# Optimization experiments

Measured on AMD Instinct MI355X. Metric: run time of the kernel, lower is better.

Reference implementation:

```python
import jax, jax.numpy as jnp
import numpy as np

I, H, L, D, O = 256, 512, 2, 2, 8  # input, hidden, layers, directions, output


def _lstm_dir(x, h0, c0, w_ih, w_hh, b, reverse):
    """One LSTM direction. x: [S,B,in] -> hidden seq [S,B,H] (time-aligned)."""
    def step(carry, xt):
        h, c = carry
        gates = xt @ w_ih.T + h @ w_hh.T + b            # [B,4H], PyTorch gate order i,f,g,o
        i, f, g, o = jnp.split(gates, 4, axis=-1)
        c = jax.nn.sigmoid(f) * c + jax.nn.sigmoid(i) * jnp.tanh(g)
        h = jax.nn.sigmoid(o) * jnp.tanh(c)
        return (h, c), h
    _, ys = jax.lax.scan(step, (h0, c0), x, reverse=reverse)
    return ys


def setup_inputs() -> dict:
    key = jax.random.key(0)
    ks = jax.random.split(key, 32)
    s = 1.0 / np.sqrt(H)
    inp = {
        "input_seq": jax.random.normal(ks[0], (64, 512, I), jnp.float32),
        "h0": jax.random.normal(ks[1], (L * D, 64, H), jnp.float32),
        "c0": jax.random.normal(ks[2], (L * D, 64, H), jnp.float32),
    }
    k = 3
    for l in range(L):
        in_dim = I if l == 0 else H * D
        for d, tag in enumerate("fb"):
            inp[f"w_ih_{l}{tag}"] = jax.random.uniform(ks[k], (4 * H, in_dim), jnp.float32, -s, s); k += 1
            inp[f"w_hh_{l}{tag}"] = jax.random.uniform(ks[k], (4 * H, H), jnp.float32, -s, s); k += 1
            inp[f"b_{l}{tag}"] = jax.random.uniform(ks[k], (4 * H,), jnp.float32, -s, s); k += 1  # b_ih + b_hh combined
    inp["fc_w"] = jax.random.uniform(ks[k], (O, H * D), jnp.float32, -s, s); k += 1
    inp["fc_b"] = jax.random.uniform(ks[k], (O,), jnp.float32, -s, s)
    return inp


def reference(input_seq, h0, c0,
              w_ih_0f, w_hh_0f, b_0f, w_ih_0b, w_hh_0b, b_0b,
              w_ih_1f, w_hh_1f, b_1f, w_ih_1b, w_hh_1b, b_1b,
              fc_w, fc_b):
    x = jnp.transpose(input_seq, (1, 0, 2))  # [S,B,I] time-major
    params = [
        ((w_ih_0f, w_hh_0f, b_0f), (w_ih_0b, w_hh_0b, b_0b)),
        ((w_ih_1f, w_hh_1f, b_1f), (w_ih_1b, w_hh_1b, b_1b)),
    ]
    for l, (pf, pb) in enumerate(params):
        fwd = _lstm_dir(x, h0[2 * l], c0[2 * l], *pf, reverse=False)
        bwd = _lstm_dir(x, h0[2 * l + 1], c0[2 * l + 1], *pb, reverse=True)
        x = jnp.concatenate([fwd, bwd], axis=-1)  # [S,B,2H]
    last = x[-1]                                   # [B,2H] == output[:, -1, :]
    pred = last @ fc_w.T + fc_b                    # fc then slice last step (same math)
    return pred[None]                              # torch.stack([pred], dim=0) -> [1,B,O]
```

## Files before the change

kernel.cpp:

```cpp
#include <hip/hip_runtime.h>
#include <hip/hip_bf16.h>


typedef __attribute__((ext_vector_type(8))) __bf16 bf16x8;
typedef __attribute__((ext_vector_type(4))) float f32x4;

struct Params {
  const float *input_seq, *h0, *c0;
  const float *w_ih_0f, *w_hh_0f, *b_0f;
  const float *w_ih_0b, *w_hh_0b, *b_0b;
  const float *w_ih_1f, *w_hh_1f, *b_1f;
  const float *w_ih_1b, *w_hh_1b, *b_1b;
  const float *fc_w, *fc_b;
  float* out;
  unsigned* flags;
  unsigned* stepf;
  __bf16* xT;
  __bf16* Wp0f; __bf16* Wp0b;
  __bf16* Wp1f; __bf16* Wp1b;
  __bf16* y0;
  __bf16* y1f;
  __bf16* h1binit;
  __bf16* h1bout;
  float* bp;
};

__device__ __forceinline__ float sigm(float x) { return 1.f / (1.f + __expf(-x)); }
__device__ __forceinline__ float tanh_fast(float x) {
  return 1.f - 2.f / (1.f + __expf(2.f * x));
}
__device__ __forceinline__ void pin(bf16x8& v) { asm volatile("" : "+v"(v)); }

__device__ __forceinline__ void phase_barrier(unsigned* pf, int wg, int tid, unsigned phase) {
  __syncthreads();
  if (tid == 0) {
    __builtin_amdgcn_fence(__ATOMIC_RELEASE, "agent");
    __hip_atomic_store(pf + wg, phase, __ATOMIC_RELAXED, __HIP_MEMORY_SCOPE_AGENT);
  }
  bool ok;
  unsigned it = 0;
  do {
    unsigned v = __hip_atomic_load(pf + tid, __ATOMIC_RELAXED, __HIP_MEMORY_SCOPE_AGENT);
    ok = (v >= phase) || (++it > 200000u);
    if (!ok) __builtin_amdgcn_s_sleep(8);
  } while (!__syncthreads_and(ok));
  __builtin_amdgcn_fence(__ATOMIC_ACQUIRE, "agent");
}

__device__ __forceinline__ bool group_wait128(const unsigned* base, int lane,
                                              unsigned need, bool fast) {
  for (unsigned it = 0;; ++it) {
    unsigned v0 = __hip_atomic_load(base + (size_t)lane * 16, __ATOMIC_RELAXED,
                                    __HIP_MEMORY_SCOPE_AGENT);
    unsigned v1 = __hip_atomic_load(base + (size_t)(lane + 64) * 16, __ATOMIC_RELAXED,
                                    __HIP_MEMORY_SCOPE_AGENT);
    bool ok = (v0 >= need) && (v1 >= need);
    if (__ballot(ok) == ~0ull) break;
    if (it > 1000000u) return false;
    if (!fast) __builtin_amdgcn_s_sleep(1);
  }
  asm volatile("" ::: "memory");
  return true;
}

__device__ __forceinline__ void flag_store(unsigned* a, unsigned v, bool fast) {
  if (fast) __hip_atomic_store(a, v, __ATOMIC_RELAXED, __HIP_MEMORY_SCOPE_WORKGROUP);
  else      __hip_atomic_store(a, v, __ATOMIC_RELAXED, __HIP_MEMORY_SCOPE_AGENT);
}

__device__ __forceinline__ void pointwise_t2(f32x4 g4, float& c,
                                             __bf16* eptr, bool fast) {
  float cj = sigm(g4[1]) * c + sigm(g4[0]) * tanh_fast(g4[2]);
  c = cj;
  float h = sigm(g4[3]) * tanh_fast(cj);
  __bf16 hb = (__bf16)h;
  unsigned short hu; __builtin_memcpy(&hu, &hb, 2);
  if (fast)
    __hip_atomic_store((unsigned short*)eptr, hu,
                       __ATOMIC_RELAXED, __HIP_MEMORY_SCOPE_WORKGROUP);
  else
    __hip_atomic_store((unsigned short*)eptr, hu,
                       __ATOMIC_RELAXED, __HIP_MEMORY_SCOPE_AGENT);
}

__global__ __launch_bounds__(256, 1) void lstm_kernel(Params p) {
  const int tid  = threadIdx.x;
  const int wg   = blockIdx.x;
  const unsigned gtid = wg * 256 + tid;
  const int lane = tid & 63;
  const int wv   = tid >> 6;
  const int colq = lane & 15;
  const int quad = lane >> 4;

  __shared__ __bf16 wlds[32768];

  {
    unsigned xcd = __builtin_amdgcn_s_getreg(20 | (31 << 11));
    if (tid == 0) p.flags[512 + wg] = xcd;
  }
  {
    int row = gtid >> 1, half = gtid & 1;
    int t = row >> 6, b = row & 63;
    const float* src = p.input_seq + ((size_t)b * 512 + t) * 256 + half * 128;
    __bf16* dst = p.xT + (size_t)row * 256 + half * 128;
    for (int i = 0; i < 128; i += 8) {
      bf16x8 v;
      #pragma unroll
      for (int j = 0; j < 8; ++j) v[j] = (__bf16)src[i + j];
      *(bf16x8*)(dst + i) = v;
    }
  }
  for (unsigned task = gtid; task < 2u * 2048 * 6; task += 65536) {
    unsigned dir = task / (2048 * 6);
    unsigned rr = (task / 6) % 2048;
    unsigned ch = task % 6;
    unsigned R = (rr & 3) * 512 + (rr >> 2);
    const float* wih = dir ? p.w_ih_0b : p.w_ih_0f;
    const float* whh = dir ? p.w_hh_0b : p.w_hh_0f;
    __bf16* dst = (dir ? p.Wp0b : p.Wp0f) + (size_t)rr * 768;
    const float* src; unsigned kd;
    if (ch < 4) { src = whh + (size_t)R * 512 + ch * 128;        kd = ch * 128; }
    else        { src = wih + (size_t)R * 256 + (ch - 4) * 128;  kd = 512 + (ch - 4) * 128; }
    for (int i = 0; i < 128; i += 8) {
      bf16x8 v;
      #pragma unroll
      for (int j = 0; j < 8; ++j) v[j] = (__bf16)src[i + j];
      *(bf16x8*)(dst + kd + i) = v;
    }
  }
  for (unsigned task = gtid; task < 2u * 2048 * 12; task += 65536) {
    unsigned dir = task / (2048 * 12);
    unsigned rr = (task / 12) % 2048;
    unsigned ch = task % 12;
    unsigned R = (rr & 3) * 512 + (rr >> 2);
    const float* wih = dir ? p.w_ih_1b : p.w_ih_1f;
    const float* whh = dir ? p.w_hh_1b : p.w_hh_1f;
    __bf16* dst = (dir ? p.Wp1b : p.Wp1f) + (size_t)rr * 1536;
    const float* src; unsigned kd;
    if (ch < 4) { src = whh + (size_t)R * 512 + ch * 128;         kd = ch * 128; }
    else        { src = wih + (size_t)R * 1024 + (ch - 4) * 128;  kd = 512 + (ch - 4) * 128; }
    for (int i = 0; i < 128; i += 8) {
      bf16x8 v;
      #pragma unroll
      for (int j = 0; j < 8; ++j) v[j] = (__bf16)src[i + j];
      *(bf16x8*)(dst + kd + i) = v;
    }
  }
  if (gtid < 4u * 2048) {
    unsigned arr = gtid >> 11, rr = gtid & 2047;
    unsigned R = (rr & 3) * 512 + (rr >> 2);
    const float* src = arr == 0 ? p.b_0f : arr == 1 ? p.b_0b : arr == 2 ? p.b_1f : p.b_1b;
    p.bp[arr * 2048 + rr] = src[R];
  }
  if (gtid < 4u * 4096) {
    unsigned dl = gtid >> 12;
    unsigned e = (gtid & 4095) * 8;
    unsigned b = e >> 9, u = e & 511;
    const float* src = p.h0 + (size_t)dl * 64 * 512 + (size_t)b * 512 + u;
    __bf16* dst;
    if (dl == 0)      dst = p.y0 + ((size_t)0 * 64 + b) * 1024 + u;
    else if (dl == 1) dst = p.y0 + ((size_t)513 * 64 + b) * 1024 + 512 + u;
    else if (dl == 2) dst = p.y1f + ((size_t)0 * 64 + b) * 512 + u;
    else              dst = p.h1binit + (size_t)b * 512 + u;
    bf16x8 v;
    #pragma unroll
    for (int j = 0; j < 8; ++j) v[j] = (__bf16)src[j];
    *(bf16x8*)dst = v;
  }

  phase_barrier(p.flags, wg, tid, 1u);

  bool fast;
  {
    const unsigned* xt = p.flags + 512;
    const int r = wg & 7;
    unsigned x0 = xt[r];
    bool ok = true;
    for (int k = 1; k < 32; ++k) ok &= (xt[r + 8 * k] == x0);
    unsigned mask = 0;
    for (int rr = 0; rr < 8; ++rr) mask |= 1u << (xt[rr] & 31);
    ok &= (__popc(mask) == 8);
    fast = ok;
  }

  {
    const int g = wg & 7;
    const bool fwd = g < 4;
    const int bg = g & 3;
    const int ug = wg >> 3;
    const int bbase = bg * 16;
    const int uglob = ug * 16 + wv * 4;
    const int colbase = uglob * 4;
    const __bf16* Wp = fwd ? p.Wp0f : p.Wp0b;
    bf16x8 wfH[16], wfI[8];
    #pragma unroll
    for (int kb = 0; kb < 16; ++kb)
      wfH[kb] = *(const bf16x8*)(Wp + (size_t)(colbase + colq) * 768 + kb * 32 + quad * 8);
    #pragma unroll
    for (int kb = 0; kb < 8; ++kb)
      wfI[kb] = *(const bf16x8*)(Wp + (size_t)(colbase + colq) * 768 + 512 + kb * 32 + quad * 8);
    #pragma unroll
    for (int kb = 0; kb < 16; ++kb) pin(wfH[kb]);
    #pragma unroll
    for (int kb = 0; kb < 8; ++kb) pin(wfI[kb]);
    const f32x4 bias4 = *(const f32x4*)(p.bp + (fwd ? 0 : 1) * 2048 + colbase + quad * 4);
    float c = p.c0[(size_t)(fwd ? 0 : 1) * 64 * 512 +
                   (size_t)(bbase + colq) * 512 + uglob + quad];
    const int dcol = fwd ? 0 : 512;
    unsigned* gfl = p.stepf + (size_t)g * 128 * 16;
    bool alive = true;
    for (int s = 0; s < 512; ++s) {
      const int t = fwd ? s : 511 - s;
      const int slabA = fwd ? t : t + 2;
      const __bf16* aX = p.xT + ((size_t)t * 64 + bbase + colq) * 256 + quad * 8;
      f32x4 accX = bias4;
      #pragma unroll
      for (int kb = 0; kb < 8; ++kb) {
        bf16x8 xv = *(const bf16x8*)(aX + kb * 32);
        accX = __builtin_amdgcn_mfma_f32_16x16x32_bf16(wfI[kb], xv, accX, 0, 0, 0);
      }
      if (s > 0 && alive) alive = group_wait128(gfl, lane, (unsigned)s, fast);
      const __bf16* aH = p.y0 + ((size_t)slabA * 64 + bbase + colq) * 1024 + dcol + quad * 8;
      f32x4 a0 = {0.f, 0.f, 0.f, 0.f}, a1 = {0.f, 0.f, 0.f, 0.f};
      f32x4 a2 = {0.f, 0.f, 0.f, 0.f}, a3 = {0.f, 0.f, 0.f, 0.f};
      #pragma unroll
      for (int kb = 0; kb < 4; ++kb) {
        a0 = __builtin_amdgcn_mfma_f32_16x16x32_bf16(wfH[kb],      *(const bf16x8*)(aH + kb * 32),        a0, 0, 0, 0);
        a1 = __builtin_amdgcn_mfma_f32_16x16x32_bf16(wfH[4 + kb],  *(const bf16x8*)(aH + (4 + kb) * 32),  a1, 0, 0, 0);
        a2 = __builtin_amdgcn_mfma_f32_16x16x32_bf16(wfH[8 + kb],  *(const bf16x8*)(aH + (8 + kb) * 32),  a2, 0, 0, 0);
        a3 = __builtin_amdgcn_mfma_f32_16x16x32_bf16(wfH[12 + kb], *(const bf16x8*)(aH + (12 + kb) * 32), a3, 0, 0, 0);
      }
      f32x4 g4 = accX + (a0 + a1) + (a2 + a3);
      pointwise_t2(g4, c,
        p.y0 + ((size_t)(t + 1) * 64 + bbase + colq) * 1024 + dcol + uglob + quad, fast);
      if (s < 511) {
        asm volatile("s_waitcnt vmcnt(0)" ::: "memory");
        if (lane == 0)
          flag_store(gfl + (size_t)(ug * 4 + wv) * 16, (unsigned)(s + 1), fast);
      }
    }
  }
  phase_barrier(p.flags, wg, tid, 2u);

  if ((wg & 7) < 4) {
    const int bg = wg & 7;
    const int ug = wg >> 3;
    const int bbase = bg * 16;
    const int uglob = ug * 16 + wv * 4;
    const int colbase = uglob * 4;
    bf16x8 wfH[16], wfX2[16];
    #pragma unroll
    for (int kb = 0; kb < 16; ++kb)
      wfH[kb] = *(const bf16x8*)(p.Wp1f + (size_t)(colbase + colq) * 1536 + kb * 32 + quad * 8);
    {
      const __bf16* wsrc = p.Wp1f + (size_t)(colbase + colq) * 1536 + 512;
      #pragma unroll
      for (int kb = 0; kb < 16; ++kb) {
        bf16x8 w = *(const bf16x8*)(wsrc + kb * 32 + quad * 8);
        *(bf16x8*)(wlds + ((size_t)(wv * 16 + kb) * 64 + lane) * 8) = w;
      }
      #pragma unroll
      for (int kb = 0; kb < 16; ++kb)
        wfX2[kb] = *(const bf16x8*)(wsrc + (16 + kb) * 32 + quad * 8);
    }
    #pragma unroll
    for (int kb = 0; kb < 16; ++kb) pin(wfH[kb]);
    #pragma unroll
    for (int kb = 0; kb < 16; ++kb) pin(wfX2[kb]);
    const f32x4 bias4 = *(const f32x4*)(p.bp + 2 * 2048 + colbase + quad * 4);
    float c = p.c0[(size_t)2 * 64 * 512 +
                   (size_t)(bbase + colq) * 512 + uglob + quad];
    unsigned* gfl = p.stepf + (size_t)(8 + bg) * 128 * 16;
    bool alive = true;
    for (int t = 0; t < 512; ++t) {
      const __bf16* aX = p.y0 + ((size_t)(t + 1) * 64 + bbase + colq) * 1024 + quad * 8;
      f32x4 accX0 = bias4, accX1 = {0.f, 0.f, 0.f, 0.f};
      #pragma unroll
      for (int kb = 0; kb < 16; ++kb) {
        bf16x8 xv = *(const bf16x8*)(aX + kb * 32);
        bf16x8 wx = *(const bf16x8*)(wlds + ((size_t)(wv * 16 + kb) * 64 + lane) * 8);
        accX0 = __builtin_amdgcn_mfma_f32_16x16x32_bf16(wx, xv, accX0, 0, 0, 0);
      }
      #pragma unroll
      for (int kb = 0; kb < 16; ++kb) {
        bf16x8 xv = *(const bf16x8*)(aX + (16 + kb) * 32);
        accX1 = __builtin_amdgcn_mfma_f32_16x16x32_bf16(wfX2[kb], xv, accX1, 0, 0, 0);
      }
      if (t > 0 && alive) alive = group_wait128(gfl, lane, (unsigned)t, fast);
      const __bf16* aH = p.y1f + ((size_t)t * 64 + bbase + colq) * 512 + quad * 8;
      f32x4 a0 = {0.f, 0.f, 0.f, 0.f}, a1 = {0.f, 0.f, 0.f, 0.f};
      f32x4 a2 = {0.f, 0.f, 0.f, 0.f}, a3 = {0.f, 0.f, 0.f, 0.f};
      #pragma unroll
      for (int kb = 0; kb < 4; ++kb) {
        a0 = __builtin_amdgcn_mfma_f32_16x16x32_bf16(wfH[kb],      *(const bf16x8*)(aH + kb * 32),        a0, 0, 0, 0);
        a1 = __builtin_amdgcn_mfma_f32_16x16x32_bf16(wfH[4 + kb],  *(const bf16x8*)(aH + (4 + kb) * 32),  a1, 0, 0, 0);
        a2 = __builtin_amdgcn_mfma_f32_16x16x32_bf16(wfH[8 + kb],  *(const bf16x8*)(aH + (8 + kb) * 32),  a2, 0, 0, 0);
        a3 = __builtin_amdgcn_mfma_f32_16x16x32_bf16(wfH[12 + kb], *(const bf16x8*)(aH + (12 + kb) * 32), a3, 0, 0, 0);
      }
      f32x4 g4 = (accX0 + accX1) + (a0 + a1) + (a2 + a3);
      pointwise_t2(g4, c,
        p.y1f + ((size_t)(t + 1) * 64 + bbase + colq) * 512 + uglob + quad, fast);
      if (t < 511) {
        asm volatile("s_waitcnt vmcnt(0)" ::: "memory");
        if (lane == 0)
          flag_store(gfl + (size_t)(ug * 4 + wv) * 16, (unsigned)(t + 1), fast);
      }
    }
  } else {
    const int bg = (wg & 7) - 4;
    const int ug = wg >> 3;
    const int bbase = bg * 16;
    const int uglob = ug * 16 + wv * 4;
    const int colbase = uglob * 4;
    const __bf16* aH = p.h1binit + (size_t)(bbase + colq) * 512 + quad * 8;
    const __bf16* aX = p.y0 + ((size_t)512 * 64 + bbase + colq) * 1024 + quad * 8;
    const __bf16* wrow = p.Wp1b + (size_t)(colbase + colq) * 1536;
    const f32x4 bias4 = *(const f32x4*)(p.bp + 3 * 2048 + colbase + quad * 4);
    f32x4 accH = bias4;
    f32x4 accX0 = {0.f, 0.f, 0.f, 0.f}, accX1 = {0.f, 0.f, 0.f, 0.f};
    #pragma unroll
    for (int kb = 0; kb < 16; ++kb)
      accH = __builtin_amdgcn_mfma_f32_16x16x32_bf16(*(const bf16x8*)(wrow + kb * 32 + quad * 8),
                                                     *(const bf16x8*)(aH + kb * 32), accH, 0, 0, 0);
    #pragma unroll
    for (int kb = 0; kb < 16; ++kb)
      accX0 = __builtin_amdgcn_mfma_f32_16x16x32_bf16(*(const bf16x8*)(wrow + (16 + kb) * 32 + quad * 8),
                                                      *(const bf16x8*)(aX + kb * 32), accX0, 0, 0, 0);
    #pragma unroll
    for (int kb = 0; kb < 16; ++kb)
      accX1 = __builtin_amdgcn_mfma_f32_16x16x32_bf16(*(const bf16x8*)(wrow + (32 + kb) * 32 + quad * 8),
                                                      *(const bf16x8*)(aX + (16 + kb) * 32), accX1, 0, 0, 0);
    f32x4 g4 = accH + accX0 + accX1;
    float c = p.c0[(size_t)3 * 64 * 512 +
                   (size_t)(bbase + colq) * 512 + uglob + quad];
    pointwise_t2(g4, c,
      p.h1bout + (size_t)(bbase + colq) * 512 + uglob + quad, true);
  }
  phase_barrier(p.flags, wg, tid, 3u);

  if (wg < 8) {
    const int b = wg * 8 + (tid >> 5);
    const int o = (tid >> 2) & 7;
    const int ks = tid & 3;
    const int k0 = ks * 256;
    const __bf16* l1 = p.y1f + ((size_t)512 * 64 + b) * 512;
    const __bf16* l2 = p.h1bout + (size_t)b * 512;
    const __bf16* hsrc = (ks < 2) ? (l1 + k0) : (l2 + k0 - 512);
    const float* w = p.fc_w + (size_t)o * 1024 + k0;
    float acc = 0.f;
    for (int k = 0; k < 256; ++k) acc += (float)hsrc[k] * w[k];
    acc += __shfl_down(acc, 2, 4);
    acc += __shfl_down(acc, 1, 4);
    if (ks == 0) p.out[b * 8 + o] = acc + p.fc_b[o];
  }
}

extern "C" void kernel_launch(void* const* d_in, const int* in_sizes, int n_in,
                              void* d_out, int out_size, void* d_ws, size_t ws_size,
                              hipStream_t stream) {
  char* ws = (char*)d_ws;
  Params p;
  p.input_seq = (const float*)d_in[0];
  p.h0 = (const float*)d_in[1];
  p.c0 = (const float*)d_in[2];
  p.w_ih_0f = (const float*)d_in[3];  p.w_hh_0f = (const float*)d_in[4];  p.b_0f = (const float*)d_in[5];
  p.w_ih_0b = (const float*)d_in[6];  p.w_hh_0b = (const float*)d_in[7];  p.b_0b = (const float*)d_in[8];
  p.w_ih_1f = (const float*)d_in[9];  p.w_hh_1f = (const float*)d_in[10]; p.b_1f = (const float*)d_in[11];
  p.w_ih_1b = (const float*)d_in[12]; p.w_hh_1b = (const float*)d_in[13]; p.b_1b = (const float*)d_in[14];
  p.fc_w = (const float*)d_in[15];    p.fc_b = (const float*)d_in[16];
  p.out = (float*)d_out;

  const size_t STEPF_BYTES = (size_t)12 * 128 * 64;
  const size_t SYNC_BYTES = 4096 + STEPF_BYTES;
  size_t off = 0;
  p.flags  = (unsigned*)(ws + off); off += 4096;
  p.stepf  = (unsigned*)(ws + off); off += STEPF_BYTES;
  p.xT     = (__bf16*)(ws + off);   off += (size_t)512 * 64 * 256 * 2;
  p.Wp0f   = (__bf16*)(ws + off);   off += (size_t)2048 * 768 * 2;
  p.Wp0b   = (__bf16*)(ws + off);   off += (size_t)2048 * 768 * 2;
  p.Wp1f   = (__bf16*)(ws + off);   off += (size_t)2048 * 1536 * 2;
  p.Wp1b   = (__bf16*)(ws + off);   off += (size_t)2048 * 1536 * 2;
  p.y0     = (__bf16*)(ws + off);   off += (size_t)514 * 64 * 1024 * 2;
  p.y1f    = (__bf16*)(ws + off);   off += (size_t)513 * 64 * 512 * 2;
  p.h1binit= (__bf16*)(ws + off);   off += (size_t)64 * 512 * 2;
  p.h1bout = (__bf16*)(ws + off);   off += (size_t)64 * 512 * 2;
  p.bp     = (float*)(ws + off);    off += (size_t)4 * 2048 * 4;
  (void)ws_size; (void)in_sizes; (void)n_in; (void)out_size;

  hipMemsetAsync(d_ws, 0, SYNC_BYTES, stream);
  lstm_kernel<<<dim3(256), dim3(256), 0, stream>>>(p);
}
```

Before: 5.510 ms.

## Replace per-step flag barriers with tagged hidden-state ring buffers

```diff
diff --git a/kernel.cpp b/kernel.cpp
--- a/kernel.cpp
+++ b/kernel.cpp
@@ -4,6 +4,7 @@
 
 typedef __attribute__((ext_vector_type(8))) __bf16 bf16x8;
 typedef __attribute__((ext_vector_type(4))) float f32x4;
+typedef __attribute__((ext_vector_type(4))) unsigned u32x4;
 
 struct Params {
   const float *input_seq, *h0, *c0;
@@ -14,12 +15,14 @@
   const float *fc_w, *fc_b;
   float* out;
   unsigned* flags;
-  unsigned* stepf;
+  unsigned* ring0f;
+  unsigned* ring0b;
+  unsigned* ring1f;
   __bf16* xT;
   __bf16* Wp0f; __bf16* Wp0b;
   __bf16* Wp1f; __bf16* Wp1b;
   __bf16* y0;
-  __bf16* y1f;
+  __bf16* h1fout;
   __bf16* h1binit;
   __bf16* h1bout;
   float* bp;
@@ -30,6 +33,20 @@
   return 1.f - 2.f / (1.f + __expf(2.f * x));
 }
 __device__ __forceinline__ void pin(bf16x8& v) { asm volatile("" : "+v"(v)); }
+
+__device__ __forceinline__ unsigned umin4(u32x4 a) {
+  unsigned m0 = a[0] < a[1] ? a[0] : a[1];
+  unsigned m1 = a[2] < a[3] ? a[2] : a[3];
+  return m0 < m1 ? m0 : m1;
+}
+__device__ __forceinline__ bf16x8 pack_lo(u32x4 a, u32x4 b) {
+  union { unsigned u[4]; bf16x8 v; } cv;
+  cv.u[0] = (a[0] & 0xffffu) | (a[1] << 16);
+  cv.u[1] = (a[2] & 0xffffu) | (a[3] << 16);
+  cv.u[2] = (b[0] & 0xffffu) | (b[1] << 16);
+  cv.u[3] = (b[2] & 0xffffu) | (b[3] << 16);
+  return cv.v;
+}
 
 __device__ __forceinline__ void phase_barrier(unsigned* pf, int wg, int tid, unsigned phase) {
   __syncthreads();
@@ -47,40 +64,18 @@
   __builtin_amdgcn_fence(__ATOMIC_ACQUIRE, "agent");
 }
 
-__device__ __forceinline__ bool group_wait128(const unsigned* base, int lane,
-                                              unsigned need, bool fast) {
-  for (unsigned it = 0;; ++it) {
-    unsigned v0 = __hip_atomic_load(base + (size_t)lane * 16, __ATOMIC_RELAXED,
-                                    __HIP_MEMORY_SCOPE_AGENT);
-    unsigned v1 = __hip_atomic_load(base + (size_t)(lane + 64) * 16, __ATOMIC_RELAXED,
-                                    __HIP_MEMORY_SCOPE_AGENT);
-    bool ok = (v0 >= need) && (v1 >= need);
-    if (__ballot(ok) == ~0ull) break;
-    if (it > 1000000u) return false;
-    if (!fast) __builtin_amdgcn_s_sleep(1);
-  }
-  asm volatile("" ::: "memory");
-  return true;
-}
-
-__device__ __forceinline__ void flag_store(unsigned* a, unsigned v, bool fast) {
-  if (fast) __hip_atomic_store(a, v, __ATOMIC_RELAXED, __HIP_MEMORY_SCOPE_WORKGROUP);
-  else      __hip_atomic_store(a, v, __ATOMIC_RELAXED, __HIP_MEMORY_SCOPE_AGENT);
-}
-
-__device__ __forceinline__ void pointwise_t2(f32x4 g4, float& c,
-                                             __bf16* eptr, bool fast) {
+__device__ __forceinline__ void ring_store(unsigned* a, unsigned v, bool fastm) {
+  if (fastm) __hip_atomic_store(a, v, __ATOMIC_RELAXED, __HIP_MEMORY_SCOPE_WORKGROUP);
+  else       __hip_atomic_store(a, v, __ATOMIC_RELAXED, __HIP_MEMORY_SCOPE_AGENT);
+}
+
+__device__ __forceinline__ unsigned short pointwise_h(f32x4 g4, float& c) {
   float cj = sigm(g4[1]) * c + sigm(g4[0]) * tanh_fast(g4[2]);
   c = cj;
   float h = sigm(g4[3]) * tanh_fast(cj);
   __bf16 hb = (__bf16)h;
   unsigned short hu; __builtin_memcpy(&hu, &hb, 2);
-  if (fast)
-    __hip_atomic_store((unsigned short*)eptr, hu,
-                       __ATOMIC_RELAXED, __HIP_MEMORY_SCOPE_WORKGROUP);
-  else
-    __hip_atomic_store((unsigned short*)eptr, hu,
-                       __ATOMIC_RELAXED, __HIP_MEMORY_SCOPE_AGENT);
+  return hu;
 }
 
 __global__ __launch_bounds__(256, 1) void lstm_kernel(Params p) {
@@ -157,15 +152,22 @@
     unsigned e = (gtid & 4095) * 8;
     unsigned b = e >> 9, u = e & 511;
     const float* src = p.h0 + (size_t)dl * 64 * 512 + (size_t)b * 512 + u;
-    __bf16* dst;
-    if (dl == 0)      dst = p.y0 + ((size_t)0 * 64 + b) * 1024 + u;
-    else if (dl == 1) dst = p.y0 + ((size_t)513 * 64 + b) * 1024 + 512 + u;
-    else if (dl == 2) dst = p.y1f + ((size_t)0 * 64 + b) * 512 + u;
-    else              dst = p.h1binit + (size_t)b * 512 + u;
-    bf16x8 v;
-    #pragma unroll
-    for (int j = 0; j < 8; ++j) v[j] = (__bf16)src[j];
-    *(bf16x8*)dst = v;
+    if (dl == 3) {
+      __bf16* dst = p.h1binit + (size_t)b * 512 + u;
+      bf16x8 v;
+      #pragma unroll
+      for (int j = 0; j < 8; ++j) v[j] = (__bf16)src[j];
+      *(bf16x8*)dst = v;
+    } else {
+      unsigned* dst = (dl == 0 ? p.ring0f : dl == 1 ? p.ring0b : p.ring1f) +
+                      ((size_t)b * 512 + u);
+      #pragma unroll
+      for (int j = 0; j < 8; ++j) {
+        __bf16 hb = (__bf16)src[j];
+        unsigned short hu; __builtin_memcpy(&hu, &hb, 2);
+        dst[j] = (unsigned)hu;
+      }
+    }
   }
 
   phase_barrier(p.flags, wg, tid, 1u);
@@ -192,6 +194,7 @@
     const int uglob = ug * 16 + wv * 4;
     const int colbase = uglob * 4;
     const __bf16* Wp = fwd ? p.Wp0f : p.Wp0b;
+    unsigned* ring = fwd ? p.ring0f : p.ring0b;
     bf16x8 wfH[16], wfI[8];
     #pragma unroll
     for (int kb = 0; kb < 16; ++kb)
@@ -207,11 +210,9 @@
     float c = p.c0[(size_t)(fwd ? 0 : 1) * 64 * 512 +
                    (size_t)(bbase + colq) * 512 + uglob + quad];
     const int dcol = fwd ? 0 : 512;
-    unsigned* gfl = p.stepf + (size_t)g * 128 * 16;
     bool alive = true;
     for (int s = 0; s < 512; ++s) {
       const int t = fwd ? s : 511 - s;
-      const int slabA = fwd ? t : t + 2;
       const __bf16* aX = p.xT + ((size_t)t * 64 + bbase + colq) * 256 + quad * 8;
       f32x4 accX = bias4;
       #pragma unroll
@@ -219,25 +220,48 @@
         bf16x8 xv = *(const bf16x8*)(aX + kb * 32);
         accX = __builtin_amdgcn_mfma_f32_16x16x32_bf16(wfI[kb], xv, accX, 0, 0, 0);
       }
-      if (s > 0 && alive) alive = group_wait128(gfl, lane, (unsigned)s, fast);
-      const __bf16* aH = p.y0 + ((size_t)slabA * 64 + bbase + colq) * 1024 + dcol + quad * 8;
+      const unsigned gtag = (unsigned)s;
+      const unsigned* rowR = ring + (((size_t)(s & 3) * 64 + bbase + colq) * 512);
+      u32x4 A[16], Bv[16];
+      unsigned lim = alive ? 100000u : 0u;
+      unsigned it = 0;
+      bool ok;
+      do {
+        #pragma unroll
+        for (int kb = 0; kb < 16; ++kb) {
+          const unsigned* pa = rowR + kb * 32 + quad * 8;
+          asm volatile("global_load_dwordx4 %0, %1, off sc1" : "=v"(A[kb]) : "v"(pa) : "memory");
+          asm volatile("global_load_dwordx4 %0, %1, off sc1" : "=v"(Bv[kb]) : "v"(pa + 4) : "memory");
+        }
+        asm volatile("s_waitcnt vmcnt(0)" ::: "memory");
+        #pragma unroll
+        for (int kb = 0; kb < 16; ++kb) asm volatile("" : "+v"(A[kb]), "+v"(Bv[kb]));
+        bool f = true;
+        #pragma unroll
+        for (int kb = 0; kb < 16; ++kb) {
+          unsigned ma = umin4(A[kb]), mb = umin4(Bv[kb]);
+          unsigned m = ma < mb ? ma : mb;
+          f &= ((m >> 16) == gtag);
+        }
+        ok = (__ballot(f) == ~0ull);
+        if (!ok && !fast) __builtin_amdgcn_s_sleep(1);
+      } while (!ok && ++it <= lim);
+      if (!ok) alive = false;
       f32x4 a0 = {0.f, 0.f, 0.f, 0.f}, a1 = {0.f, 0.f, 0.f, 0.f};
       f32x4 a2 = {0.f, 0.f, 0.f, 0.f}, a3 = {0.f, 0.f, 0.f, 0.f};
       #pragma unroll
       for (int kb = 0; kb < 4; ++kb) {
-        a0 = __builtin_amdgcn_mfma_f32_16x16x32_bf16(wfH[kb],      *(const bf16x8*)(aH + kb * 32),        a0, 0, 0, 0);
-        a1 = __builtin_amdgcn_mfma_f32_16x16x32_bf16(wfH[4 + kb],  *(const bf16x8*)(aH + (4 + kb) * 32),  a1, 0, 0, 0);
-        a2 = __builtin_amdgcn_mfma_f32_16x16x32_bf16(wfH[8 + kb],  *(const bf16x8*)(aH + (8 + kb) * 32),  a2, 0, 0, 0);
-        a3 = __builtin_amdgcn_mfma_f32_16x16x32_bf16(wfH[12 + kb], *(const bf16x8*)(aH + (12 + kb) * 32), a3, 0, 0, 0);
+        a0 = __builtin_amdgcn_mfma_f32_16x16x32_bf16(wfH[kb],      pack_lo(A[kb],      Bv[kb]),      a0, 0, 0, 0);
+        a1 = __builtin_amdgcn_mfma_f32_16x16x32_bf16(wfH[4 + kb],  pack_lo(A[4 + kb],  Bv[4 + kb]),  a1, 0, 0, 0);
+        a2 = __builtin_amdgcn_mfma_f32_16x16x32_bf16(wfH[8 + kb],  pack_lo(A[8 + kb],  Bv[8 + kb]),  a2, 0, 0, 0);
+        a3 = __builtin_amdgcn_mfma_f32_16x16x32_bf16(wfH[12 + kb], pack_lo(A[12 + kb], Bv[12 + kb]), a3, 0, 0, 0);
       }
       f32x4 g4 = accX + (a0 + a1) + (a2 + a3);
-      pointwise_t2(g4, c,
-        p.y0 + ((size_t)(t + 1) * 64 + bbase + colq) * 1024 + dcol + uglob + quad, fast);
-      if (s < 511) {
-        asm volatile("s_waitcnt vmcnt(0)" ::: "memory");
-        if (lane == 0)
-          flag_store(gfl + (size_t)(ug * 4 + wv) * 16, (unsigned)(s + 1), fast);
-      }
+      unsigned short hu = pointwise_h(g4, c);
+      ring_store(ring + (((size_t)((s + 1) & 3) * 64 + bbase + colq) * 512 + uglob + quad),
+                 ((unsigned)(s + 1) << 16) | (unsigned)hu, fast);
+      __hip_atomic_store((unsigned short*)(p.y0 + ((size_t)(t + 1) * 64 + bbase + colq) * 1024 + dcol + uglob + quad),
+                         hu, __ATOMIC_RELAXED, __HIP_MEMORY_SCOPE_WORKGROUP);
     }
   }
   phase_barrier(p.flags, wg, tid, 2u);
@@ -270,7 +294,6 @@
     const f32x4 bias4 = *(const f32x4*)(p.bp + 2 * 2048 + colbase + quad * 4);
     float c = p.c0[(size_t)2 * 64 * 512 +
                    (size_t)(bbase + colq) * 512 + uglob + quad];
-    unsigned* gfl = p.stepf + (size_t)(8 + bg) * 128 * 16;
     bool alive = true;
     for (int t = 0; t < 512; ++t) {
       const __bf16* aX = p.y0 + ((size_t)(t + 1) * 64 + bbase + colq) * 1024 + quad * 8;
@@ -286,25 +309,49 @@
         bf16x8 xv = *(const bf16x8*)(aX + (16 + kb) * 32);
         accX1 = __builtin_amdgcn_mfma_f32_16x16x32_bf16(wfX2[kb], xv, accX1, 0, 0, 0);
       }
-      if (t > 0 && alive) alive = group_wait128(gfl, lane, (unsigned)t, fast);
-      const __bf16* aH = p.y1f + ((size_t)t * 64 + bbase + colq) * 512 + quad * 8;
+      const unsigned gtag = (unsigned)t;
+      const unsigned* rowR = p.ring1f + (((size_t)(t & 3) * 64 + bbase + colq) * 512);
+      u32x4 A[16], Bv[16];
+      unsigned lim = alive ? 100000u : 0u;
+      unsigned it = 0;
+      bool ok;
+      do {
+        #pragma unroll
+        for (int kb = 0; kb < 16; ++kb) {
+          const unsigned* pa = rowR + kb * 32 + quad * 8;
+          asm volatile("global_load_dwordx4 %0, %1, off sc1" : "=v"(A[kb]) : "v"(pa) : "memory");
+          asm volatile("global_load_dwordx4 %0, %1, off sc1" : "=v"(Bv[kb]) : "v"(pa + 4) : "memory");
+        }
+        asm volatile("s_waitcnt vmcnt(0)" ::: "memory");
+        #pragma unroll
+        for (int kb = 0; kb < 16; ++kb) asm volatile("" : "+v"(A[kb]), "+v"(Bv[kb]));
+        bool f = true;
+        #pragma unroll
+        for (int kb = 0; kb < 16; ++kb) {
+          unsigned ma = umin4(A[kb]), mb = umin4(Bv[kb]);
+          unsigned m = ma < mb ? ma : mb;
+          f &= ((m >> 16) == gtag);
+        }
+        ok = (__ballot(f) == ~0ull);
+        if (!ok && !fast) __builtin_amdgcn_s_sleep(1);
+      } while (!ok && ++it <= lim);
+      if (!ok) alive = false;
       f32x4 a0 = {0.f, 0.f, 0.f, 0.f}, a1 = {0.f, 0.f, 0.f, 0.f};
       f32x4 a2 = {0.f, 0.f, 0.f, 0.f}, a3 = {0.f, 0.f, 0.f, 0.f};
       #pragma unroll
       for (int kb = 0; kb < 4; ++kb) {
-        a0 = __builtin_amdgcn_mfma_f32_16x16x32_bf16(wfH[kb],      *(const bf16x8*)(aH + kb * 32),        a0, 0, 0, 0);
-        a1 = __builtin_amdgcn_mfma_f32_16x16x32_bf16(wfH[4 + kb],  *(const bf16x8*)(aH + (4 + kb) * 32),  a1, 0, 0, 0);
-        a2 = __builtin_amdgcn_mfma_f32_16x16x32_bf16(wfH[8 + kb],  *(const bf16x8*)(aH + (8 + kb) * 32),  a2, 0, 0, 0);
-        a3 = __builtin_amdgcn_mfma_f32_16x16x32_bf16(wfH[12 + kb], *(const bf16x8*)(aH + (12 + kb) * 32), a3, 0, 0, 0);
+        a0 = __builtin_amdgcn_mfma_f32_16x16x32_bf16(wfH[kb],      pack_lo(A[kb],      Bv[kb]),      a0, 0, 0, 0);
+        a1 = __builtin_amdgcn_mfma_f32_16x16x32_bf16(wfH[4 + kb],  pack_lo(A[4 + kb],  Bv[4 + kb]),  a1, 0, 0, 0);
+        a2 = __builtin_amdgcn_mfma_f32_16x16x32_bf16(wfH[8 + kb],  pack_lo(A[8 + kb],  Bv[8 + kb]),  a2, 0, 0, 0);
+        a3 = __builtin_amdgcn_mfma_f32_16x16x32_bf16(wfH[12 + kb], pack_lo(A[12 + kb], Bv[12 + kb]), a3, 0, 0, 0);
       }
       f32x4 g4 = (accX0 + accX1) + (a0 + a1) + (a2 + a3);
-      pointwise_t2(g4, c,
-        p.y1f + ((size_t)(t + 1) * 64 + bbase + colq) * 512 + uglob + quad, fast);
-      if (t < 511) {
-        asm volatile("s_waitcnt vmcnt(0)" ::: "memory");
-        if (lane == 0)
-          flag_store(gfl + (size_t)(ug * 4 + wv) * 16, (unsigned)(t + 1), fast);
-      }
+      unsigned short hu = pointwise_h(g4, c);
+      ring_store(p.ring1f + (((size_t)((t + 1) & 3) * 64 + bbase + colq) * 512 + uglob + quad),
+                 ((unsigned)(t + 1) << 16) | (unsigned)hu, fast);
+      if (t == 511)
+        __hip_atomic_store((unsigned short*)(p.h1fout + (size_t)(bbase + colq) * 512 + uglob + quad),
+                           hu, __ATOMIC_RELAXED, __HIP_MEMORY_SCOPE_WORKGROUP);
     }
   } else {
     const int bg = (wg & 7) - 4;
@@ -333,8 +380,9 @@
     f32x4 g4 = accH + accX0 + accX1;
     float c = p.c0[(size_t)3 * 64 * 512 +
                    (size_t)(bbase + colq) * 512 + uglob + quad];
-    pointwise_t2(g4, c,
-      p.h1bout + (size_t)(bbase + colq) * 512 + uglob + quad, true);
+    unsigned short hu = pointwise_h(g4, c);
+    __hip_atomic_store((unsigned short*)(p.h1bout + (size_t)(bbase + colq) * 512 + uglob + quad),
+                       hu, __ATOMIC_RELAXED, __HIP_MEMORY_SCOPE_WORKGROUP);
   }
   phase_barrier(p.flags, wg, tid, 3u);
 
@@ -343,7 +391,7 @@
     const int o = (tid >> 2) & 7;
     const int ks = tid & 3;
     const int k0 = ks * 256;
-    const __bf16* l1 = p.y1f + ((size_t)512 * 64 + b) * 512;
+    const __bf16* l1 = p.h1fout + (size_t)b * 512;
     const __bf16* l2 = p.h1bout + (size_t)b * 512;
     const __bf16* hsrc = (ks < 2) ? (l1 + k0) : (l2 + k0 - 512);
     const float* w = p.fc_w + (size_t)o * 1024 + k0;
@@ -370,18 +418,20 @@
   p.fc_w = (const float*)d_in[15];    p.fc_b = (const float*)d_in[16];
   p.out = (float*)d_out;
 
-  const size_t STEPF_BYTES = (size_t)12 * 128 * 64;
-  const size_t SYNC_BYTES = 4096 + STEPF_BYTES;
+  const size_t RING_BYTES = (size_t)4 * 64 * 512 * 4;
+  const size_t SYNC_BYTES = 4096 + 3 * RING_BYTES;
   size_t off = 0;
   p.flags  = (unsigned*)(ws + off); off += 4096;
-  p.stepf  = (unsigned*)(ws + off); off += STEPF_BYTES;
+  p.ring0f = (unsigned*)(ws + off); off += RING_BYTES;
+  p.ring0b = (unsigned*)(ws + off); off += RING_BYTES;
+  p.ring1f = (unsigned*)(ws + off); off += RING_BYTES;
   p.xT     = (__bf16*)(ws + off);   off += (size_t)512 * 64 * 256 * 2;
   p.Wp0f   = (__bf16*)(ws + off);   off += (size_t)2048 * 768 * 2;
   p.Wp0b   = (__bf16*)(ws + off);   off += (size_t)2048 * 768 * 2;
   p.Wp1f   = (__bf16*)(ws + off);   off += (size_t)2048 * 1536 * 2;
   p.Wp1b   = (__bf16*)(ws + off);   off += (size_t)2048 * 1536 * 2;
   p.y0     = (__bf16*)(ws + off);   off += (size_t)514 * 64 * 1024 * 2;
-  p.y1f    = (__bf16*)(ws + off);   off += (size_t)513 * 64 * 512 * 2;
+  p.h1fout = (__bf16*)(ws + off);   off += (size_t)64 * 512 * 2;
   p.h1binit= (__bf16*)(ws + off);   off += (size_t)64 * 512 * 2;
   p.h1bout = (__bf16*)(ws + off);   off += (size_t)64 * 512 * 2;
   p.bp     = (float*)(ws + off);    off += (size_t)4 * 2048 * 4;
```

Result: slower. 8.063 ms (+46.3%).
